# Kernel tuning notes

Measured on AMD Instinct MI355X. Metric: run time of the kernel, lower is better.

Reference implementation:

```python
import jax, jax.numpy as jnp
import numpy as np

EMBED = 1024
HEADS = 16
HEAD_DIM = EMBED // HEADS
LN_EPS = 1e-5


def setup_inputs() -> dict:
    key = jax.random.key(0)
    ks = jax.random.split(key, 7)
    B, S = 2, 2048
    x = jax.random.normal(ks[0], (B, S, EMBED), dtype=jnp.float32)
    attn_params = jax.random.uniform(ks[1], (B, S, 3 * EMBED), dtype=jnp.float32)
    sc = 1.0 / np.sqrt(EMBED)
    Wqkv = jax.random.normal(ks[2], (3 * EMBED, EMBED), dtype=jnp.float32) * sc
    Wout = jax.random.normal(ks[3], (EMBED, EMBED), dtype=jnp.float32) * sc
    b_out = jnp.zeros((EMBED,), dtype=jnp.float32)
    gamma = jnp.ones((EMBED,), dtype=jnp.float32)
    beta = jnp.zeros((EMBED,), dtype=jnp.float32)
    return {"x": x, "attn_params": attn_params, "Wqkv": Wqkv, "Wout": Wout,
            "b_out": b_out, "gamma": gamma, "beta": beta}


def reference(x, attn_params, Wqkv, Wout, b_out, gamma, beta):
    B, S, E = x.shape
    # qkv projection (no bias) followed by elementwise attn_params scaling
    qkv = jnp.einsum('bse,fe->bsf', x, Wqkv) * attn_params  # [B,S,3E]
    q, k, v = jnp.split(qkv, 3, axis=-1)
    # [B,H,S,D]
    q = q.reshape(B, S, HEADS, HEAD_DIM).transpose(0, 2, 1, 3)
    k = k.reshape(B, S, HEADS, HEAD_DIM).transpose(0, 2, 1, 3)
    v = v.reshape(B, S, HEADS, HEAD_DIM).transpose(0, 2, 1, 3)
    scores = jnp.einsum('bhqd,bhkd->bhqk', q, k) / jnp.sqrt(jnp.float32(HEAD_DIM))
    attn = jax.nn.softmax(scores, axis=-1)
    weighted = jnp.einsum('bhqk,bhkd->bhqd', attn, v)  # [B,H,S,D]
    weighted = weighted.transpose(0, 2, 1, 3).reshape(B, S, E)
    out = jnp.einsum('bse,fe->bsf', weighted, Wout) + b_out
    out = out + x  # residual
    # layernorm over last dim
    mu = jnp.mean(out, axis=-1, keepdims=True)
    var = jnp.mean(jnp.square(out - mu), axis=-1, keepdims=True)
    return (out - mu) * jax.lax.rsqrt(var + LN_EPS) * gamma + beta
```

## Files before the change

### kernel.cpp

```cpp
#include <hip/hip_runtime.h>

typedef float f32x4 __attribute__((ext_vector_type(4)));
typedef short s16x8 __attribute__((ext_vector_type(8)));
typedef unsigned short u16;

#define AS1 __attribute__((address_space(1)))
#define AS3 __attribute__((address_space(3)))

__device__ __forceinline__ u16 f2bf(float f){
    union { float f; unsigned u; } v; v.f = f;
    unsigned r = v.u + 0x7FFFu + ((v.u >> 16) & 1u);
    return (u16)(r >> 16);
}

__device__ __forceinline__ void pswap(unsigned &A, unsigned &B){
    asm("v_permlane32_swap_b32 %0, %1\n\tv_permlane16_swap_b32 %0, %1" : "+v"(A), "+v"(B));
}
__device__ __forceinline__ unsigned cvtpk(float lo, float hi){
    unsigned w;
    asm("v_cvt_pk_bf16_f32 %0, %1, %2" : "=v"(w) : "v"(lo), "v"(hi));
    return w;
}

__global__ __launch_bounds__(256) void cvt3_bf16(
    const float* __restrict__ a, u16* __restrict__ da, int na,
    const float* __restrict__ b, u16* __restrict__ db, int nb,
    const float* __restrict__ c, u16* __restrict__ dc, int nc)
{
    int i = blockIdx.x * 256 + threadIdx.x;
    const float* s; u16* d; int off;
    if (i < na){ s = a; d = da; off = i; }
    else if (i < na + nb){ s = b; d = db; off = i - na; }
    else if (i < na + nb + nc){ s = c; d = dc; off = i - na - nb; }
    else return;
    float4 v = ((const float4*)s)[off];
    ushort4 o;
    o.x = f2bf(v.x); o.y = f2bf(v.y); o.z = f2bf(v.z); o.w = f2bf(v.w);
    ((ushort4*)d)[off] = o;
}

__global__ __launch_bounds__(512, 2) void gemm256(
    const u16* __restrict__ A, const u16* __restrict__ Bw,
    int N, int K,
    const float* __restrict__ e0, u16* __restrict__ Cout)
{
    __shared__ u16 lds[2][4][128 * 64];
    const int tid = threadIdx.x;
    const int w = tid >> 6, l = tid & 63;
    const int g = l >> 4, c = l & 15;
    const int wm = w >> 2, wn = w & 3;
    const int nbh = 2 + (wn >> 1);
    const int nb = wn & 1;
    const int sg = (g ^ (((c >> 3) & 1) << 1) ^ ((c >> 2) & 1)) << 4;

    const int bid = blockIdx.x;
    const int xcd = bid & 7, lin = bid >> 3;
    const int rowBase = (xcd * 2 + (lin & 1)) * 256;
    const int colBase = (lin >> 1) * 256;

    const int s_r_lo = l >> 2;
    const int s_col  = ((l & 3) ^ (((l >> 5) & 1) << 1) ^ ((l >> 4) & 1)) * 8;

    f32x4 acc[8][4] = {};

#define STAGE_HALF(bb, hh, j_) do{                                                         \
    const u16* Gb_ = ((hh) < 2) ? (A + (size_t)(rowBase + (hh) * 128) * K)                 \
                                : (Bw + (size_t)(colBase + ((hh) - 2) * 128) * K);         \
    _Pragma("unroll")                                                                      \
    for (int i_ = 0; i_ < 2; ++i_){                                                        \
        int st_ = i_ * 8 + w;                                                              \
        int r_  = (st_ >> 1) * 16 + s_r_lo;                                                \
        int col_ = (st_ & 1) * 32 + s_col;                                                 \
        const u16* src_ = Gb_ + (size_t)r_ * K + ((j_) * 64 + col_);                       \
        __builtin_amdgcn_global_load_lds((const AS1 void*)src_,                            \
            (AS3 void*)((char*)&lds[bb][hh][0] + (i_ * 8 + w) * 1024), 16, 0, 0);          \
    } }while(0)

#define LDA4(bb, mh) do{                                                                   \
    _Pragma("unroll") for (int mi_ = 0; mi_ < 4; ++mi_){                                   \
        _Pragma("unroll") for (int kk_ = 0; kk_ < 2; ++kk_){                               \
            int mt_ = (mh) * 4 + mi_;                                                      \
            a2[mi_][kk_] = *(const s16x8*)((const char*)&lds[bb][wm][0] +                  \
                (((mt_ * 2 + kk_) << 10) + c * 64 + sg));                                  \
        } } }while(0)

#define LDB2(bb, nh) do{                                                                   \
    _Pragma("unroll") for (int ni_ = 0; ni_ < 2; ++ni_){                                   \
        _Pragma("unroll") for (int kk_ = 0; kk_ < 2; ++kk_){                               \
            int nt_ = (nh) * 2 + ni_;                                                      \
            bfr[nh][ni_][kk_] = *(const s16x8*)((const char*)&lds[bb][nbh][0] +            \
                ((((nb * 4 + nt_) * 2 + kk_) << 10) + c * 64 + sg));                       \
        } } }while(0)

#define MFMA16(mh, nh) do{                                                                 \
    __builtin_amdgcn_s_setprio(1);                                                         \
    _Pragma("unroll") for (int mi_ = 0; mi_ < 4; ++mi_){                                   \
        _Pragma("unroll") for (int ni_ = 0; ni_ < 2; ++ni_){                               \
            _Pragma("unroll") for (int kk_ = 0; kk_ < 2; ++kk_){                           \
                acc[(mh)*4+mi_][(nh)*2+ni_] = __builtin_amdgcn_mfma_f32_16x16x32_bf16(     \
                    a2[mi_][kk_], bfr[nh][ni_][kk_], acc[(mh)*4+mi_][(nh)*2+ni_], 0,0,0);  \
            } } }                                                                          \
    __builtin_amdgcn_s_setprio(0);                                                         \
}while(0)

    const int ntk = K >> 6;
    STAGE_HALF(0, 0, 0); STAGE_HALF(0, 1, 0); STAGE_HALF(0, 2, 0); STAGE_HALF(0, 3, 0);
    __syncthreads();

    s16x8 a2[4][2];
    s16x8 bfr[2][2][2];
    for (int j = 0; j < ntk; ++j){
        const int cur = j & 1, nxt = cur ^ 1;
        const bool pf = (j + 1 < ntk);
        LDA4(cur, 0);
        LDB2(cur, 0);
        if (pf){ STAGE_HALF(nxt, 0, j + 1); STAGE_HALF(nxt, 1, j + 1); }
        MFMA16(0, 0);
        LDB2(cur, 1);
        if (pf) STAGE_HALF(nxt, 2, j + 1);
        MFMA16(0, 1);
        LDA4(cur, 1);
        if (pf) STAGE_HALF(nxt, 3, j + 1);
        MFMA16(1, 1);
        MFMA16(1, 0);
        __syncthreads();
    }

#pragma unroll
    for (int mt = 0; mt < 8; ++mt){
        const int rbase = rowBase + wm * 128 + mt * 16 + g * 4;
        float ev[16];
#pragma unroll
        for (int nt_ = 0; nt_ < 4; ++nt_){
            const int cc = colBase + wn * 64 + nt_ * 16 + c;
#pragma unroll
            for (int jj = 0; jj < 4; ++jj)
                ev[nt_ * 4 + jj] = e0[(size_t)(rbase + jj) * N + cc];
        }
#pragma unroll
        for (int nt_ = 0; nt_ < 4; ++nt_){
            const int cc = colBase + wn * 64 + nt_ * 16 + c;
#pragma unroll
            for (int jj = 0; jj < 4; ++jj){
                float apv = ev[nt_ * 4 + jj];
                if (cc < 1024) apv *= 0.18033688f;
                Cout[(size_t)(rbase + jj) * N + cc] = f2bf(acc[mt][nt_][jj] * apv);
            }
        }
    }
#undef STAGE_HALF
#undef LDA4
#undef LDB2
#undef MFMA16
}

__global__ __launch_bounds__(256) void gemm_bt(
    const u16* __restrict__ A, const u16* __restrict__ Bw,
    int M, int N, int K,
    const float* __restrict__ e0, const float* __restrict__ e1,
    float* __restrict__ Cout)
{
    __shared__ u16 As[2][128 * 32];
    __shared__ u16 Bs[2][128 * 32];
    const int tid = threadIdx.x;
    const int w = tid >> 6, lane = tid & 63;
    const int g = lane >> 4, c = lane & 15;
    const int wr = w >> 1, wc = w & 1;
    const int rowBase = blockIdx.y * 128;
    const int colBase = blockIdx.x * 128;

    f32x4 acc[4][4] = {};

    auto STAGE = [&](int pb, int k0){
#pragma unroll
        for (int i = 0; i < 2; ++i){
            int o  = i * 4096 + tid * 16;
            int r  = o >> 6;
            int ce = (o & 63) >> 1;
            const u16* ga = A  + (size_t)(rowBase + r) * K + (k0 + ce);
            __builtin_amdgcn_global_load_lds((const AS1 void*)ga,
                (AS3 void*)((char*)As[pb] + i * 4096 + w * 1024), 16, 0, 0);
            const u16* gb = Bw + (size_t)(colBase + r) * K + (k0 + ce);
            __builtin_amdgcn_global_load_lds((const AS1 void*)gb,
                (AS3 void*)((char*)Bs[pb] + i * 4096 + w * 1024), 16, 0, 0);
        }
    };

    const int nt = K >> 5;
    STAGE(0, 0);
    __syncthreads();

    for (int t = 0; t < nt; ++t){
        const int cur = t & 1;
        if (t + 1 < nt) STAGE(cur ^ 1, (t + 1) * 32);

        s16x8 af[4], bfr[4];
#pragma unroll
        for (int m = 0; m < 4; ++m){
            int row = wr * 64 + m * 16 + c;
            af[m] = *(const s16x8*)((const char*)As[cur] + row * 64 + g * 16);
        }
#pragma unroll
        for (int n = 0; n < 4; ++n){
            int row = wc * 64 + n * 16 + c;
            bfr[n] = *(const s16x8*)((const char*)Bs[cur] + row * 64 + g * 16);
        }
#pragma unroll
        for (int m = 0; m < 4; ++m)
#pragma unroll
            for (int n = 0; n < 4; ++n)
                acc[m][n] = __builtin_amdgcn_mfma_f32_16x16x32_bf16(af[m], bfr[n], acc[m][n], 0, 0, 0);
        __syncthreads();
    }

    float bcol[4];
#pragma unroll
    for (int n = 0; n < 4; ++n)
        bcol[n] = e0[colBase + wc * 64 + n * 16 + c];

#pragma unroll
    for (int m = 0; m < 4; ++m){
        const int rbase = rowBase + wr * 64 + m * 16 + g * 4;
        float ev[16];
#pragma unroll
        for (int n = 0; n < 4; ++n){
            const int cc = colBase + wc * 64 + n * 16 + c;
#pragma unroll
            for (int j = 0; j < 4; ++j)
                ev[n * 4 + j] = e1[(size_t)(rbase + j) * N + cc];
        }
#pragma unroll
        for (int n = 0; n < 4; ++n){
            const int cc = colBase + wc * 64 + n * 16 + c;
#pragma unroll
            for (int j = 0; j < 4; ++j)
                Cout[(size_t)(rbase + j) * N + cc] = acc[m][n][j] + bcol[n] + ev[n * 4 + j];
        }
    }
}

__global__ __launch_bounds__(256) void vtrans(const u16* __restrict__ qkv, u16* __restrict__ vt){
    __shared__ u16 t_[64 * 64];
    int bh = blockIdx.x; int b = bh >> 4; int h = bh & 15;
    int st = blockIdx.y;
    int tid = threadIdx.x;
#pragma unroll
    for (int i = 0; i < 2; ++i){
        int id = i * 256 + tid;
        int sr = id >> 3, c8 = id & 7;
        uint4 v = *(const uint4*)(qkv + (size_t)(b * 2048 + st * 64 + sr) * 3072 + 2048 + h * 64 + c8 * 8);
        *(uint4*)((char*)t_ + ((sr * 128 + c8 * 16) ^ ((sr & 7) << 4))) = v;
    }
    __syncthreads();
#pragma unroll
    for (int i = 0; i < 2; ++i){
        int id = i * 256 + tid;
        int d = id >> 3, s8 = (id & 7) * 8;
        u16 tmp[8];
#pragma unroll
        for (int jj = 0; jj < 8; ++jj){
            int s = s8 + jj;
            tmp[jj] = *(const u16*)((const char*)t_ + ((s * 128 + d * 2) ^ ((s & 7) << 4)));
        }
        *(uint4*)(vt + ((size_t)bh * 64 + d) * 2048 + st * 64 + s8) = *(uint4*)tmp;
    }
}

__global__ __launch_bounds__(512) void attn_k(const u16* __restrict__ qkv,
                                              const u16* __restrict__ vt,
                                              u16* __restrict__ o)
{
    __shared__ u16 Kl[2][64 * 64];
    __shared__ u16 Vl[2][64 * 64];
    int bh = blockIdx.x; int b = bh >> 4, h = bh & 15;
    int qt = blockIdx.y;
    int tid = threadIdx.x;
    int w = tid >> 6, lane = tid & 63, g = lane >> 4, c = lane & 15;

    const size_t qrow = (size_t)(b * 2048 + qt * 128 + w * 16 + c);
    s16x8 qf[2];
    qf[0] = *(const s16x8*)(qkv + qrow * 3072 + h * 64 + g * 8);
    qf[1] = *(const s16x8*)(qkv + qrow * 3072 + h * 64 + 32 + g * 8);

    const s16x8 ones8 = {16256, 16256, 16256, 16256, 16256, 16256, 16256, 16256};

    f32x4 oa[4] = {};
    f32x4 la = {};

    int kr = tid >> 3, c8 = tid & 7;
    const u16* kg = qkv + (size_t)(b * 2048 + kr) * 3072 + 1024 + h * 64 + c8 * 8;
    const u16* vg = vt + ((size_t)bh * 64 + kr) * 2048 + c8 * 8;
    const int so = (kr * 128 + c8 * 16) ^ ((kr & 7) << 4);

    uint4 ks = *(const uint4*)kg;
    uint4 vs = *(const uint4*)vg;
    *(uint4*)((char*)Kl[0] + so) = ks;
    *(uint4*)((char*)Vl[0] + so) = vs;
    __syncthreads();

    for (int t = 0; t < 32; ++t){
        const int cur = t & 1;
        if (t < 31){
            ks = *(const uint4*)(kg + (size_t)(t + 1) * 64 * 3072);
            vs = *(const uint4*)(vg + (t + 1) * 64);
        }

        f32x4 st[4];
        __builtin_amdgcn_s_setprio(1);
#pragma unroll
        for (int kt = 0; kt < 4; ++kt){
            int row = kt * 16 + c;
            s16x8 kf0 = *(const s16x8*)((const char*)Kl[cur] + ((row * 128 + g * 16) ^ ((row & 7) << 4)));
            s16x8 kf1 = *(const s16x8*)((const char*)Kl[cur] + ((row * 128 + 64 + g * 16) ^ ((row & 7) << 4)));
            f32x4 a = {};
            a = __builtin_amdgcn_mfma_f32_16x16x32_bf16(kf0, qf[0], a, 0, 0, 0);
            a = __builtin_amdgcn_mfma_f32_16x16x32_bf16(kf1, qf[1], a, 0, 0, 0);
            st[kt] = a;
        }
        __builtin_amdgcn_s_setprio(0);

        unsigned W[4][2];
#pragma unroll
        for (int kt = 0; kt < 4; ++kt){
            float p0 = __builtin_amdgcn_exp2f(st[kt][0]);
            float p1 = __builtin_amdgcn_exp2f(st[kt][1]);
            float p2 = __builtin_amdgcn_exp2f(st[kt][2]);
            float p3 = __builtin_amdgcn_exp2f(st[kt][3]);
            W[kt][0] = cvtpk(p0, p1);
            W[kt][1] = cvtpk(p2, p3);
        }

        __builtin_amdgcn_s_setprio(1);
#pragma unroll
        for (int kb = 0; kb < 2; ++kb){
            unsigned t0 = W[kb * 2][0], t2 = W[kb * 2 + 1][0];
            pswap(t0, t2);
            unsigned t1 = W[kb * 2][1], t3 = W[kb * 2 + 1][1];
            pswap(t1, t3);
            union { unsigned u[4]; s16x8 v; } pu;
            pu.u[0] = t0; pu.u[1] = t1; pu.u[2] = t2; pu.u[3] = t3;
#pragma unroll
            for (int dt = 0; dt < 4; ++dt){
                int vrow = dt * 16 + c;
                s16x8 vf = *(const s16x8*)((const char*)Vl[cur] + ((vrow * 128 + kb * 64 + g * 16) ^ ((vrow & 7) << 4)));
                oa[dt] = __builtin_amdgcn_mfma_f32_16x16x32_bf16(vf, pu.v, oa[dt], 0, 0, 0);
            }
            la = __builtin_amdgcn_mfma_f32_16x16x32_bf16(ones8, pu.v, la, 0, 0, 0);
        }
        __builtin_amdgcn_s_setprio(0);

        if (t < 31){
            *(uint4*)((char*)Kl[cur ^ 1] + so) = ks;
            *(uint4*)((char*)Vl[cur ^ 1] + so) = vs;
        }
        __syncthreads();
    }

    float inv = 1.0f / la[0];
#pragma unroll
    for (int dt = 0; dt < 4; ++dt){
        u16 t4[4];
#pragma unroll
        for (int j = 0; j < 4; ++j) t4[j] = f2bf(oa[dt][j] * inv);
        *(uint2*)(o + qrow * 1024 + h * 64 + dt * 16 + g * 4) = *(uint2*)t4;
    }
}

__global__ __launch_bounds__(256) void ln_k(const float* __restrict__ tmp,
                                            const float* __restrict__ gamma,
                                            const float* __restrict__ beta,
                                            float* __restrict__ out)
{
    int row = blockIdx.x;
    int tid = threadIdx.x;
    float4 v = ((const float4*)(tmp + (size_t)row * 1024))[tid];
    float s  = v.x + v.y + v.z + v.w;
    float ss = v.x * v.x + v.y * v.y + v.z * v.z + v.w * v.w;
    for (int m = 1; m < 64; m <<= 1){ s += __shfl_xor(s, m); ss += __shfl_xor(ss, m); }
    __shared__ float red[8];
    int w = tid >> 6;
    if ((tid & 63) == 0){ red[w * 2] = s; red[w * 2 + 1] = ss; }
    __syncthreads();
    s  = red[0] + red[2] + red[4] + red[6];
    ss = red[1] + red[3] + red[5] + red[7];
    float mu  = s * (1.f / 1024.f);
    float var = ss * (1.f / 1024.f) - mu * mu;
    float inv = rsqrtf(var + 1e-5f);
    float4 g4 = ((const float4*)gamma)[tid];
    float4 b4 = ((const float4*)beta)[tid];
    float4 r;
    r.x = (v.x - mu) * inv * g4.x + b4.x;
    r.y = (v.y - mu) * inv * g4.y + b4.y;
    r.z = (v.z - mu) * inv * g4.z + b4.z;
    r.w = (v.w - mu) * inv * g4.w + b4.w;
    ((float4*)(out + (size_t)row * 1024))[tid] = r;
}

extern "C" void kernel_launch(void* const* d_in, const int* in_sizes, int n_in,
                              void* d_out, int out_size, void* d_ws, size_t ws_size,
                              hipStream_t stream)
{
    const float* x     = (const float*)d_in[0];
    const float* ap    = (const float*)d_in[1];
    const float* wqkv  = (const float*)d_in[2];
    const float* wout  = (const float*)d_in[3];
    const float* bout  = (const float*)d_in[4];
    const float* gamma = (const float*)d_in[5];
    const float* beta  = (const float*)d_in[6];
    float* out = (float*)d_out;

    char* ws = (char*)d_ws;
    u16* xb    = (u16*)ws;  ws += (size_t)4096 * 1024 * 2;
    u16* wqkvb = (u16*)ws;  ws += (size_t)3072 * 1024 * 2;
    u16* woutb = (u16*)ws;  ws += (size_t)1024 * 1024 * 2;
    u16* qkvb  = (u16*)ws;  ws += (size_t)4096 * 3072 * 2;
    u16* vtb   = (u16*)ws;  ws += (size_t)32 * 64 * 2048 * 2;
    u16* attnb = (u16*)ws;  ws += (size_t)4096 * 1024 * 2;
    float* tmp = (float*)ws;

    const int na = 4096 * 1024 / 4, nb = 3072 * 1024 / 4, nc = 1024 * 1024 / 4;
    cvt3_bf16<<<(na + nb + nc + 255) / 256, 256, 0, stream>>>(x, xb, na, wqkv, wqkvb, nb, wout, woutb, nc);

    gemm256<<<192, 512, 0, stream>>>(xb, wqkvb, 3072, 1024, ap, qkvb);
    vtrans<<<dim3(32, 32), 256, 0, stream>>>(qkvb, vtb);
    attn_k<<<dim3(32, 16), 512, 0, stream>>>(qkvb, vtb, attnb);
    gemm_bt<<<dim3(8, 32), 256, 0, stream>>>(attnb, woutb, 4096, 1024, 1024, bout, x, tmp);
    ln_k<<<4096, 256, 0, stream>>>(tmp, gamma, beta, out);
}
```

Before: 127.9 us.

## Restructure QKV GEMM into 8-wave ping-pong schedule with two-deep prefetch

Changes the 256x256 bf16 QKV GEMM main loop so that global-to-LDS loads run two K-tiles ahead instead of one, and each quarter of the LDS buffer is refilled as soon as it has been consumed. It also remaps which LDS quarters hold which rows, so that all waves share quarter tiles, and replaces __syncthreads with raw s_barrier plus explicit vmcnt waits. The aim is to hide global load latency and to interleave MFMA phases across waves. In exchange it adds many more barriers per iteration and relies on hand-placed waitcnt counts for correctness.

```diff
diff --git a/kernel.cpp b/kernel.cpp
--- a/kernel.cpp
+++ b/kernel.cpp
@@ -49,8 +49,6 @@
     const int w = tid >> 6, l = tid & 63;
     const int g = l >> 4, c = l & 15;
     const int wm = w >> 2, wn = w & 3;
-    const int nbh = 2 + (wn >> 1);
-    const int nb = wn & 1;
     const int sg = (g ^ (((c >> 3) & 1) << 1) ^ ((c >> 2) & 1)) << 4;
 
     const int bid = blockIdx.x;
@@ -63,36 +61,48 @@
 
     f32x4 acc[8][4] = {};
 
-#define STAGE_HALF(bb, hh, j_) do{                                                         \
-    const u16* Gb_ = ((hh) < 2) ? (A + (size_t)(rowBase + (hh) * 128) * K)                 \
-                                : (Bw + (size_t)(colBase + ((hh) - 2) * 128) * K);         \
+#define SBAR() asm volatile("s_barrier" ::: "memory")
+#define VMW(n) asm volatile("s_waitcnt vmcnt(" #n ")" ::: "memory")
+
+#define STAGE_A(bb, r, j_) do{                                                             \
     _Pragma("unroll")                                                                      \
     for (int i_ = 0; i_ < 2; ++i_){                                                        \
         int st_ = i_ * 8 + w;                                                              \
-        int r_  = (st_ >> 1) * 16 + s_r_lo;                                                \
+        int rg_ = st_ >> 1;                                                                \
+        int row_ = (rg_ >> 2) * 128 + (r) * 64 + (rg_ & 3) * 16 + s_r_lo;                  \
         int col_ = (st_ & 1) * 32 + s_col;                                                 \
-        const u16* src_ = Gb_ + (size_t)r_ * K + ((j_) * 64 + col_);                       \
+        const u16* src_ = A + (size_t)(rowBase + row_) * K + ((j_) * 64 + col_);           \
         __builtin_amdgcn_global_load_lds((const AS1 void*)src_,                            \
-            (AS3 void*)((char*)&lds[bb][hh][0] + (i_ * 8 + w) * 1024), 16, 0, 0);          \
+            (AS3 void*)((char*)&lds[bb][r][0] + st_ * 1024), 16, 0, 0);                    \
     } }while(0)
 
-#define LDA4(bb, mh) do{                                                                   \
+#define STAGE_B(bb, s, j_) do{                                                             \
+    _Pragma("unroll")                                                                      \
+    for (int i_ = 0; i_ < 2; ++i_){                                                        \
+        int st_ = i_ * 8 + w;                                                              \
+        int rg_ = st_ >> 1;                                                                \
+        int row_ = (rg_ >> 1) * 64 + (s) * 32 + (rg_ & 1) * 16 + s_r_lo;                   \
+        int col_ = (st_ & 1) * 32 + s_col;                                                 \
+        const u16* src_ = Bw + (size_t)(colBase + row_) * K + ((j_) * 64 + col_);          \
+        __builtin_amdgcn_global_load_lds((const AS1 void*)src_,                            \
+            (AS3 void*)((char*)&lds[bb][2 + (s)][0] + st_ * 1024), 16, 0, 0);              \
+    } }while(0)
+
+#define LDA(bb, mh) do{                                                                    \
     _Pragma("unroll") for (int mi_ = 0; mi_ < 4; ++mi_){                                   \
         _Pragma("unroll") for (int kk_ = 0; kk_ < 2; ++kk_){                               \
-            int mt_ = (mh) * 4 + mi_;                                                      \
-            a2[mi_][kk_] = *(const s16x8*)((const char*)&lds[bb][wm][0] +                  \
-                (((mt_ * 2 + kk_) << 10) + c * 64 + sg));                                  \
+            a2[mi_][kk_] = *(const s16x8*)((const char*)&lds[bb][mh][0] +                  \
+                ((((wm * 4 + mi_) * 2 + kk_) << 10) + c * 64 + sg));                       \
         } } }while(0)
 
-#define LDB2(bb, nh) do{                                                                   \
+#define LDB(bb, nh) do{                                                                    \
     _Pragma("unroll") for (int ni_ = 0; ni_ < 2; ++ni_){                                   \
         _Pragma("unroll") for (int kk_ = 0; kk_ < 2; ++kk_){                               \
-            int nt_ = (nh) * 2 + ni_;                                                      \
-            bfr[nh][ni_][kk_] = *(const s16x8*)((const char*)&lds[bb][nbh][0] +            \
-                ((((nb * 4 + nt_) * 2 + kk_) << 10) + c * 64 + sg));                       \
+            bfr[nh][ni_][kk_] = *(const s16x8*)((const char*)&lds[bb][2 + (nh)][0] +       \
+                ((((wn * 2 + ni_) * 2 + kk_) << 10) + c * 64 + sg));                       \
         } } }while(0)
 
-#define MFMA16(mh, nh) do{                                                                 \
+#define MFMAQ(mh, nh) do{                                                                  \
     __builtin_amdgcn_s_setprio(1);                                                         \
     _Pragma("unroll") for (int mi_ = 0; mi_ < 4; ++mi_){                                   \
         _Pragma("unroll") for (int ni_ = 0; ni_ < 2; ++ni_){                               \
@@ -104,26 +114,46 @@
 }while(0)
 
     const int ntk = K >> 6;
-    STAGE_HALF(0, 0, 0); STAGE_HALF(0, 1, 0); STAGE_HALF(0, 2, 0); STAGE_HALF(0, 3, 0);
-    __syncthreads();
+
+    STAGE_A(0, 0, 0); STAGE_B(0, 0, 0); STAGE_B(0, 1, 0); STAGE_A(0, 1, 0);
+    STAGE_A(1, 0, 1); STAGE_B(1, 0, 1); STAGE_B(1, 1, 1); STAGE_A(1, 1, 1);
+    VMW(8);
+    SBAR();
 
     s16x8 a2[4][2];
     s16x8 bfr[2][2][2];
-    for (int j = 0; j < ntk; ++j){
-        const int cur = j & 1, nxt = cur ^ 1;
-        const bool pf = (j + 1 < ntk);
-        LDA4(cur, 0);
-        LDB2(cur, 0);
-        if (pf){ STAGE_HALF(nxt, 0, j + 1); STAGE_HALF(nxt, 1, j + 1); }
-        MFMA16(0, 0);
-        LDB2(cur, 1);
-        if (pf) STAGE_HALF(nxt, 2, j + 1);
-        MFMA16(0, 1);
-        LDA4(cur, 1);
-        if (pf) STAGE_HALF(nxt, 3, j + 1);
-        MFMA16(1, 1);
-        MFMA16(1, 0);
-        __syncthreads();
+#pragma unroll 2
+    for (int t = 0; t < ntk; ++t){
+        const int cur = t & 1;
+        const bool pf = (t + 2 < ntk);
+
+        LDA(cur, 0);
+        LDB(cur, 0);
+        SBAR();
+        MFMAQ(0, 0);
+        SBAR();
+
+        LDB(cur, 1);
+        if (pf) STAGE_A(cur, 0, t + 2);
+        SBAR();
+        MFMAQ(0, 1);
+        SBAR();
+
+        LDA(cur, 1);
+        if (pf) STAGE_B(cur, 0, t + 2);
+        SBAR();
+        MFMAQ(1, 0);
+        SBAR();
+
+        if (pf){ STAGE_A(cur, 1, t + 2); STAGE_B(cur, 1, t + 2); }
+        SBAR();
+        MFMAQ(1, 1);
+        SBAR();
+
+        if (t + 1 < ntk){
+            if (pf) VMW(8); else VMW(0);
+            SBAR();
+        }
     }
 
 #pragma unroll
@@ -148,10 +178,13 @@
             }
         }
     }
-#undef STAGE_HALF
-#undef LDA4
-#undef LDB2
-#undef MFMA16
+#undef STAGE_A
+#undef STAGE_B
+#undef LDA
+#undef LDB
+#undef MFMAQ
+#undef SBAR
+#undef VMW
 }
 
 __global__ __launch_bounds__(256) void gemm_bt(
```

New measurement: 136.2 us. 6.4% more time.

## Replace 256x256 QKV GEMM with simpler 128x128-tile kernel over more blocks

Applied to the files above, without the earlier changes.

Replaces the QKV projection kernel, which used 256x256 tiles, 512 threads, K-step 64, swizzled LDS and interleaved prefetch/MFMA phases, with a 128x128-tile, 256-thread kernel using K-step 32 and a plain double-buffered loop. The grid grows from 192 to 768 blocks, spreading the work across more CUs with better occupancy and load balance. The cost is lower data reuse per block, more global traffic, and unswizzled LDS reads that may cause bank conflicts.

```diff
diff --git a/kernel.cpp b/kernel.cpp
--- a/kernel.cpp
+++ b/kernel.cpp
@@ -39,119 +39,89 @@
     ((ushort4*)d)[off] = o;
 }
 
-__global__ __launch_bounds__(512, 2) void gemm256(
+__global__ __launch_bounds__(256) void gemm128_qkv(
     const u16* __restrict__ A, const u16* __restrict__ Bw,
     int N, int K,
     const float* __restrict__ e0, u16* __restrict__ Cout)
 {
-    __shared__ u16 lds[2][4][128 * 64];
+    __shared__ u16 As[2][128 * 32];
+    __shared__ u16 Bs[2][128 * 32];
     const int tid = threadIdx.x;
-    const int w = tid >> 6, l = tid & 63;
-    const int g = l >> 4, c = l & 15;
-    const int wm = w >> 2, wn = w & 3;
-    const int nbh = 2 + (wn >> 1);
-    const int nb = wn & 1;
-    const int sg = (g ^ (((c >> 3) & 1) << 1) ^ ((c >> 2) & 1)) << 4;
+    const int w = tid >> 6, lane = tid & 63;
+    const int g = lane >> 4, c = lane & 15;
+    const int wr = w >> 1, wc = w & 1;
 
     const int bid = blockIdx.x;
     const int xcd = bid & 7, lin = bid >> 3;
-    const int rowBase = (xcd * 2 + (lin & 1)) * 256;
-    const int colBase = (lin >> 1) * 256;
-
-    const int s_r_lo = l >> 2;
-    const int s_col  = ((l & 3) ^ (((l >> 5) & 1) << 1) ^ ((l >> 4) & 1)) * 8;
-
-    f32x4 acc[8][4] = {};
-
-#define STAGE_HALF(bb, hh, j_) do{                                                         \
-    const u16* Gb_ = ((hh) < 2) ? (A + (size_t)(rowBase + (hh) * 128) * K)                 \
-                                : (Bw + (size_t)(colBase + ((hh) - 2) * 128) * K);         \
-    _Pragma("unroll")                                                                      \
-    for (int i_ = 0; i_ < 2; ++i_){                                                        \
-        int st_ = i_ * 8 + w;                                                              \
-        int r_  = (st_ >> 1) * 16 + s_r_lo;                                                \
-        int col_ = (st_ & 1) * 32 + s_col;                                                 \
-        const u16* src_ = Gb_ + (size_t)r_ * K + ((j_) * 64 + col_);                       \
-        __builtin_amdgcn_global_load_lds((const AS1 void*)src_,                            \
-            (AS3 void*)((char*)&lds[bb][hh][0] + (i_ * 8 + w) * 1024), 16, 0, 0);          \
-    } }while(0)
-
-#define LDA4(bb, mh) do{                                                                   \
-    _Pragma("unroll") for (int mi_ = 0; mi_ < 4; ++mi_){                                   \
-        _Pragma("unroll") for (int kk_ = 0; kk_ < 2; ++kk_){                               \
-            int mt_ = (mh) * 4 + mi_;                                                      \
-            a2[mi_][kk_] = *(const s16x8*)((const char*)&lds[bb][wm][0] +                  \
-                (((mt_ * 2 + kk_) << 10) + c * 64 + sg));                                  \
-        } } }while(0)
-
-#define LDB2(bb, nh) do{                                                                   \
-    _Pragma("unroll") for (int ni_ = 0; ni_ < 2; ++ni_){                                   \
-        _Pragma("unroll") for (int kk_ = 0; kk_ < 2; ++kk_){                               \
-            int nt_ = (nh) * 2 + ni_;                                                      \
-            bfr[nh][ni_][kk_] = *(const s16x8*)((const char*)&lds[bb][nbh][0] +            \
-                ((((nb * 4 + nt_) * 2 + kk_) << 10) + c * 64 + sg));                       \
-        } } }while(0)
-
-#define MFMA16(mh, nh) do{                                                                 \
-    __builtin_amdgcn_s_setprio(1);                                                         \
-    _Pragma("unroll") for (int mi_ = 0; mi_ < 4; ++mi_){                                   \
-        _Pragma("unroll") for (int ni_ = 0; ni_ < 2; ++ni_){                               \
-            _Pragma("unroll") for (int kk_ = 0; kk_ < 2; ++kk_){                           \
-                acc[(mh)*4+mi_][(nh)*2+ni_] = __builtin_amdgcn_mfma_f32_16x16x32_bf16(     \
-                    a2[mi_][kk_], bfr[nh][ni_][kk_], acc[(mh)*4+mi_][(nh)*2+ni_], 0,0,0);  \
-            } } }                                                                          \
-    __builtin_amdgcn_s_setprio(0);                                                         \
-}while(0)
-
-    const int ntk = K >> 6;
-    STAGE_HALF(0, 0, 0); STAGE_HALF(0, 1, 0); STAGE_HALF(0, 2, 0); STAGE_HALF(0, 3, 0);
-    __syncthreads();
-
-    s16x8 a2[4][2];
-    s16x8 bfr[2][2][2];
-    for (int j = 0; j < ntk; ++j){
-        const int cur = j & 1, nxt = cur ^ 1;
-        const bool pf = (j + 1 < ntk);
-        LDA4(cur, 0);
-        LDB2(cur, 0);
-        if (pf){ STAGE_HALF(nxt, 0, j + 1); STAGE_HALF(nxt, 1, j + 1); }
-        MFMA16(0, 0);
-        LDB2(cur, 1);
-        if (pf) STAGE_HALF(nxt, 2, j + 1);
-        MFMA16(0, 1);
-        LDA4(cur, 1);
-        if (pf) STAGE_HALF(nxt, 3, j + 1);
-        MFMA16(1, 1);
-        MFMA16(1, 0);
+    const int rowBase = (xcd * 4 + (lin & 3)) * 128;
+    const int colBase = (lin >> 2) * 128;
+
+    f32x4 acc[4][4] = {};
+
+    auto STAGE = [&](int pb, int k0){
+#pragma unroll
+        for (int i = 0; i < 2; ++i){
+            int o  = i * 4096 + tid * 16;
+            int r  = o >> 6;
+            int ce = (o & 63) >> 1;
+            const u16* ga = A  + (size_t)(rowBase + r) * K + (k0 + ce);
+            __builtin_amdgcn_global_load_lds((const AS1 void*)ga,
+                (AS3 void*)((char*)As[pb] + i * 4096 + w * 1024), 16, 0, 0);
+            const u16* gb = Bw + (size_t)(colBase + r) * K + (k0 + ce);
+            __builtin_amdgcn_global_load_lds((const AS1 void*)gb,
+                (AS3 void*)((char*)Bs[pb] + i * 4096 + w * 1024), 16, 0, 0);
+        }
+    };
+
+    const int nt = K >> 5;
+    STAGE(0, 0);
+    __syncthreads();
+
+    for (int t = 0; t < nt; ++t){
+        const int cur = t & 1;
+        if (t + 1 < nt) STAGE(cur ^ 1, (t + 1) * 32);
+
+        s16x8 af[4], bfr[4];
+#pragma unroll
+        for (int m = 0; m < 4; ++m){
+            int row = wr * 64 + m * 16 + c;
+            af[m] = *(const s16x8*)((const char*)As[cur] + row * 64 + g * 16);
+        }
+#pragma unroll
+        for (int n = 0; n < 4; ++n){
+            int row = wc * 64 + n * 16 + c;
+            bfr[n] = *(const s16x8*)((const char*)Bs[cur] + row * 64 + g * 16);
+        }
+#pragma unroll
+        for (int m = 0; m < 4; ++m)
+#pragma unroll
+            for (int n = 0; n < 4; ++n)
+                acc[m][n] = __builtin_amdgcn_mfma_f32_16x16x32_bf16(af[m], bfr[n], acc[m][n], 0, 0, 0);
         __syncthreads();
     }
 
 #pragma unroll
-    for (int mt = 0; mt < 8; ++mt){
-        const int rbase = rowBase + wm * 128 + mt * 16 + g * 4;
+    for (int m = 0; m < 4; ++m){
+        const int rbase = rowBase + wr * 64 + m * 16 + g * 4;
         float ev[16];
 #pragma unroll
-        for (int nt_ = 0; nt_ < 4; ++nt_){
-            const int cc = colBase + wn * 64 + nt_ * 16 + c;
-#pragma unroll
-            for (int jj = 0; jj < 4; ++jj)
-                ev[nt_ * 4 + jj] = e0[(size_t)(rbase + jj) * N + cc];
-        }
-#pragma unroll
-        for (int nt_ = 0; nt_ < 4; ++nt_){
-            const int cc = colBase + wn * 64 + nt_ * 16 + c;
-#pragma unroll
-            for (int jj = 0; jj < 4; ++jj){
-                float apv = ev[nt_ * 4 + jj];
+        for (int n = 0; n < 4; ++n){
+            const int cc = colBase + wc * 64 + n * 16 + c;
+#pragma unroll
+            for (int j = 0; j < 4; ++j)
+                ev[n * 4 + j] = e0[(size_t)(rbase + j) * N + cc];
+        }
+#pragma unroll
+        for (int n = 0; n < 4; ++n){
+            const int cc = colBase + wc * 64 + n * 16 + c;
+#pragma unroll
+            for (int j = 0; j < 4; ++j){
+                float apv = ev[n * 4 + j];
                 if (cc < 1024) apv *= 0.18033688f;
-                Cout[(size_t)(rbase + jj) * N + cc] = f2bf(acc[mt][nt_][jj] * apv);
+                Cout[(size_t)(rbase + j) * N + cc] = f2bf(acc[m][n][j] * apv);
             }
         }
     }
-#undef STAGE_HALF
-#undef LDA4
-#undef LDB2
-#undef MFMA16
 }
 
 __global__ __launch_bounds__(256) void gemm_bt(
@@ -421,7 +391,7 @@
     const int na = 4096 * 1024 / 4, nb = 3072 * 1024 / 4, nc = 1024 * 1024 / 4;
     cvt3_bf16<<<(na + nb + nc + 255) / 256, 256, 0, stream>>>(x, xb, na, wqkv, wqkvb, nb, wout, woutb, nc);
 
-    gemm256<<<192, 512, 0, stream>>>(xb, wqkvb, 3072, 1024, ap, qkvb);
+    gemm128_qkv<<<768, 256, 0, stream>>>(xb, wqkvb, 3072, 1024, ap, qkvb);
     vtrans<<<dim3(32, 32), 256, 0, stream>>>(qkvb, vtb);
     attn_k<<<dim3(32, 16), 512, 0, stream>>>(qkvb, vtb, attnb);
     gemm_bt<<<dim3(8, 32), 256, 0, stream>>>(attnb, woutb, 4096, 1024, 1024, bout, x, tmp);
```

Result: slower. 141.9 us (+10.9%).

## Process two 16-row query tiles per wave in attention with 256 threads

Applied to the files above, without the earlier changes.

The attention kernel drops from 8 to 4 waves per block, and each wave now handles 32 query rows (two 16-row sub-tiles) instead of 16. Each K and V fragment read from LDS is reused across both sub-tiles, halving LDS reads per MFMA, and each thread now loads two K and V vectors per tile. The cost is roughly double the accumulator and score registers per wave, which may lower occupancy, and fewer waves are left per block to hide latency.

```diff
diff --git a/kernel.cpp b/kernel.cpp
--- a/kernel.cpp
+++ b/kernel.cpp
@@ -266,7 +266,7 @@
     }
 }
 
-__global__ __launch_bounds__(512) void attn_k(const u16* __restrict__ qkv,
+__global__ __launch_bounds__(256) void attn_k(const u16* __restrict__ qkv,
                                               const u16* __restrict__ vt,
                                               u16* __restrict__ o)
 {
@@ -277,92 +277,118 @@
     int tid = threadIdx.x;
     int w = tid >> 6, lane = tid & 63, g = lane >> 4, c = lane & 15;
 
-    const size_t qrow = (size_t)(b * 2048 + qt * 128 + w * 16 + c);
-    s16x8 qf[2];
-    qf[0] = *(const s16x8*)(qkv + qrow * 3072 + h * 64 + g * 8);
-    qf[1] = *(const s16x8*)(qkv + qrow * 3072 + h * 64 + 32 + g * 8);
+    const size_t qrow0 = (size_t)(b * 2048 + qt * 128 + w * 32 + c);
+    const size_t qrow1 = qrow0 + 16;
+    s16x8 qf[2][2];
+    qf[0][0] = *(const s16x8*)(qkv + qrow0 * 3072 + h * 64 + g * 8);
+    qf[0][1] = *(const s16x8*)(qkv + qrow0 * 3072 + h * 64 + 32 + g * 8);
+    qf[1][0] = *(const s16x8*)(qkv + qrow1 * 3072 + h * 64 + g * 8);
+    qf[1][1] = *(const s16x8*)(qkv + qrow1 * 3072 + h * 64 + 32 + g * 8);
 
     const s16x8 ones8 = {16256, 16256, 16256, 16256, 16256, 16256, 16256, 16256};
 
-    f32x4 oa[4] = {};
-    f32x4 la = {};
+    f32x4 oa[2][4] = {};
+    f32x4 la[2] = {};
 
     int kr = tid >> 3, c8 = tid & 7;
     const u16* kg = qkv + (size_t)(b * 2048 + kr) * 3072 + 1024 + h * 64 + c8 * 8;
     const u16* vg = vt + ((size_t)bh * 64 + kr) * 2048 + c8 * 8;
-    const int so = (kr * 128 + c8 * 16) ^ ((kr & 7) << 4);
-
-    uint4 ks = *(const uint4*)kg;
-    uint4 vs = *(const uint4*)vg;
-    *(uint4*)((char*)Kl[0] + so) = ks;
-    *(uint4*)((char*)Vl[0] + so) = vs;
+    const int so0 = (kr * 128 + c8 * 16) ^ ((kr & 7) << 4);
+    const int so1 = so0 + 32 * 128;
+
+    uint4 ks0 = *(const uint4*)kg;
+    uint4 ks1 = *(const uint4*)(kg + (size_t)32 * 3072);
+    uint4 vs0 = *(const uint4*)vg;
+    uint4 vs1 = *(const uint4*)(vg + (size_t)32 * 2048);
+    *(uint4*)((char*)Kl[0] + so0) = ks0;
+    *(uint4*)((char*)Kl[0] + so1) = ks1;
+    *(uint4*)((char*)Vl[0] + so0) = vs0;
+    *(uint4*)((char*)Vl[0] + so1) = vs1;
     __syncthreads();
 
     for (int t = 0; t < 32; ++t){
         const int cur = t & 1;
         if (t < 31){
-            ks = *(const uint4*)(kg + (size_t)(t + 1) * 64 * 3072);
-            vs = *(const uint4*)(vg + (t + 1) * 64);
-        }
-
-        f32x4 st[4];
+            ks0 = *(const uint4*)(kg + (size_t)(t + 1) * 64 * 3072);
+            ks1 = *(const uint4*)(kg + (size_t)(t + 1) * 64 * 3072 + (size_t)32 * 3072);
+            vs0 = *(const uint4*)(vg + (t + 1) * 64);
+            vs1 = *(const uint4*)(vg + (t + 1) * 64 + (size_t)32 * 2048);
+        }
+
+        f32x4 st[2][4];
         __builtin_amdgcn_s_setprio(1);
 #pragma unroll
         for (int kt = 0; kt < 4; ++kt){
             int row = kt * 16 + c;
             s16x8 kf0 = *(const s16x8*)((const char*)Kl[cur] + ((row * 128 + g * 16) ^ ((row & 7) << 4)));
             s16x8 kf1 = *(const s16x8*)((const char*)Kl[cur] + ((row * 128 + 64 + g * 16) ^ ((row & 7) << 4)));
-            f32x4 a = {};
-            a = __builtin_amdgcn_mfma_f32_16x16x32_bf16(kf0, qf[0], a, 0, 0, 0);
-            a = __builtin_amdgcn_mfma_f32_16x16x32_bf16(kf1, qf[1], a, 0, 0, 0);
-            st[kt] = a;
+#pragma unroll
+            for (int qh = 0; qh < 2; ++qh){
+                f32x4 a = {};
+                a = __builtin_amdgcn_mfma_f32_16x16x32_bf16(kf0, qf[qh][0], a, 0, 0, 0);
+                a = __builtin_amdgcn_mfma_f32_16x16x32_bf16(kf1, qf[qh][1], a, 0, 0, 0);
+                st[qh][kt] = a;
+            }
         }
         __builtin_amdgcn_s_setprio(0);
 
-        unsigned W[4][2];
+        unsigned W[2][4][2];
+#pragma unroll
+        for (int qh = 0; qh < 2; ++qh)
 #pragma unroll
         for (int kt = 0; kt < 4; ++kt){
-            float p0 = __builtin_amdgcn_exp2f(st[kt][0]);
-            float p1 = __builtin_amdgcn_exp2f(st[kt][1]);
-            float p2 = __builtin_amdgcn_exp2f(st[kt][2]);
-            float p3 = __builtin_amdgcn_exp2f(st[kt][3]);
-            W[kt][0] = cvtpk(p0, p1);
-            W[kt][1] = cvtpk(p2, p3);
+            float p0 = __builtin_amdgcn_exp2f(st[qh][kt][0]);
+            float p1 = __builtin_amdgcn_exp2f(st[qh][kt][1]);
+            float p2 = __builtin_amdgcn_exp2f(st[qh][kt][2]);
+            float p3 = __builtin_amdgcn_exp2f(st[qh][kt][3]);
+            W[qh][kt][0] = cvtpk(p0, p1);
+            W[qh][kt][1] = cvtpk(p2, p3);
         }
 
         __builtin_amdgcn_s_setprio(1);
 #pragma unroll
         for (int kb = 0; kb < 2; ++kb){
-            unsigned t0 = W[kb * 2][0], t2 = W[kb * 2 + 1][0];
-            pswap(t0, t2);
-            unsigned t1 = W[kb * 2][1], t3 = W[kb * 2 + 1][1];
-            pswap(t1, t3);
-            union { unsigned u[4]; s16x8 v; } pu;
-            pu.u[0] = t0; pu.u[1] = t1; pu.u[2] = t2; pu.u[3] = t3;
+            union { unsigned u[4]; s16x8 v; } pu[2];
+#pragma unroll
+            for (int qh = 0; qh < 2; ++qh){
+                unsigned t0 = W[qh][kb * 2][0], t2 = W[qh][kb * 2 + 1][0];
+                pswap(t0, t2);
+                unsigned t1 = W[qh][kb * 2][1], t3 = W[qh][kb * 2 + 1][1];
+                pswap(t1, t3);
+                pu[qh].u[0] = t0; pu[qh].u[1] = t1; pu[qh].u[2] = t2; pu[qh].u[3] = t3;
+            }
 #pragma unroll
             for (int dt = 0; dt < 4; ++dt){
                 int vrow = dt * 16 + c;
                 s16x8 vf = *(const s16x8*)((const char*)Vl[cur] + ((vrow * 128 + kb * 64 + g * 16) ^ ((vrow & 7) << 4)));
-                oa[dt] = __builtin_amdgcn_mfma_f32_16x16x32_bf16(vf, pu.v, oa[dt], 0, 0, 0);
+                oa[0][dt] = __builtin_amdgcn_mfma_f32_16x16x32_bf16(vf, pu[0].v, oa[0][dt], 0, 0, 0);
+                oa[1][dt] = __builtin_amdgcn_mfma_f32_16x16x32_bf16(vf, pu[1].v, oa[1][dt], 0, 0, 0);
             }
-            la = __builtin_amdgcn_mfma_f32_16x16x32_bf16(ones8, pu.v, la, 0, 0, 0);
+            la[0] = __builtin_amdgcn_mfma_f32_16x16x32_bf16(ones8, pu[0].v, la[0], 0, 0, 0);
+            la[1] = __builtin_amdgcn_mfma_f32_16x16x32_bf16(ones8, pu[1].v, la[1], 0, 0, 0);
         }
         __builtin_amdgcn_s_setprio(0);
 
         if (t < 31){
-            *(uint4*)((char*)Kl[cur ^ 1] + so) = ks;
-            *(uint4*)((char*)Vl[cur ^ 1] + so) = vs;
+            *(uint4*)((char*)Kl[cur ^ 1] + so0) = ks0;
+            *(uint4*)((char*)Kl[cur ^ 1] + so1) = ks1;
+            *(uint4*)((char*)Vl[cur ^ 1] + so0) = vs0;
+            *(uint4*)((char*)Vl[cur ^ 1] + so1) = vs1;
         }
         __syncthreads();
     }
 
-    float inv = 1.0f / la[0];
-#pragma unroll
-    for (int dt = 0; dt < 4; ++dt){
-        u16 t4[4];
-#pragma unroll
-        for (int j = 0; j < 4; ++j) t4[j] = f2bf(oa[dt][j] * inv);
-        *(uint2*)(o + qrow * 1024 + h * 64 + dt * 16 + g * 4) = *(uint2*)t4;
+#pragma unroll
+    for (int qh = 0; qh < 2; ++qh){
+        const size_t qr = (qh == 0) ? qrow0 : qrow1;
+        float inv = 1.0f / la[qh][0];
+#pragma unroll
+        for (int dt = 0; dt < 4; ++dt){
+            u16 t4[4];
+#pragma unroll
+            for (int j = 0; j < 4; ++j) t4[j] = f2bf(oa[qh][dt][j] * inv);
+            *(uint2*)(o + qr * 1024 + h * 64 + dt * 16 + g * 4) = *(uint2*)t4;
+        }
     }
 }
 
@@ -423,7 +449,7 @@
 
     gemm256<<<192, 512, 0, stream>>>(xb, wqkvb, 3072, 1024, ap, qkvb);
     vtrans<<<dim3(32, 32), 256, 0, stream>>>(qkvb, vtb);
-    attn_k<<<dim3(32, 16), 512, 0, stream>>>(qkvb, vtb, attnb);
+    attn_k<<<dim3(32, 16), 256, 0, stream>>>(qkvb, vtb, attnb);
     gemm_bt<<<dim3(8, 32), 256, 0, stream>>>(attnb, woutb, 4096, 1024, 1024, bout, x, tmp);
     ln_k<<<4096, 256, 0, stream>>>(tmp, gamma, beta, out);
 }
```

New measurement: 132.4 us. 3.5% more time.
